# Kernel optimization log

Measured on AMD Instinct MI355X. Metric: run time of the kernel, lower is better.

## Reference

```python
import jax, jax.numpy as jnp
import numpy as np

HEAD_SIZE = 64


def setup_inputs() -> dict:
    key = jax.random.key(0)
    kx, kq, kk, kv = jax.random.split(key, 4)
    B, L, D = 4, 4096, 1024
    scale = 1.0 / np.sqrt(D)
    x = jax.random.normal(kx, (B, L, D), dtype=jnp.float32)
    Wq = jax.random.normal(kq, (D, HEAD_SIZE), dtype=jnp.float32) * scale
    Wk = jax.random.normal(kk, (D, HEAD_SIZE), dtype=jnp.float32) * scale
    Wv = jax.random.normal(kv, (D, HEAD_SIZE), dtype=jnp.float32) * scale
    return {"x": x, "Wq": Wq, "Wk": Wk, "Wv": Wv}


def reference(x, Wq, Wk, Wv):
    B, L, D = x.shape
    H = Wq.shape[1]
    q = jnp.einsum('bld,dh->blh', x, Wq)  # [B,L,H]
    k = jnp.einsum('bld,dh->blh', x, Wk)
    v = jnp.einsum('bld,dh->blh', x, Wv)
    # full L x L score matrix, as in the original module
    scores = jnp.einsum('bqh,bkh->bqk', q, k) / jnp.sqrt(jnp.float32(H))
    causal = jnp.tril(jnp.ones((L, L), dtype=bool))
    scores = jnp.where(causal, scores, -jnp.inf)
    attn = jax.nn.softmax(scores, axis=-1)
    z = jnp.einsum('bqk,bkh->bqh', attn, v)  # [B,L,H]
    return z
```

## Files before the change

### kernel.cpp

```cpp
#include <hip/hip_runtime.h>
#include <stdint.h>

#define L_SEQ 4096
#define D_MODEL 1024
#define HEAD 64
#define CHUNK 512
#define MAXCH 8
#define NQT 128

typedef unsigned short u16;
typedef __attribute__((ext_vector_type(8))) short bf16x8;
typedef __attribute__((ext_vector_type(4))) float f32x4;

static __device__ __forceinline__ u16 f2bf(float f) {
    union { float f; uint32_t u; } c; c.f = f;
    uint32_t u = c.u;
    return (u16)((u + 0x7FFFu + ((u >> 16) & 1u)) >> 16);
}
static __device__ __forceinline__ bf16x8 ld8(const u16* p) { return *(const bf16x8*)p; }

static __device__ __forceinline__ f32x4 mfma16(bf16x8 a, bf16x8 b, f32x4 c) {
    return __builtin_amdgcn_mfma_f32_16x16x32_bf16(a, b, c, 0, 0, 0);
}

__global__ __launch_bounds__(256) void conv_w(
    const float* __restrict__ Wq, const float* __restrict__ Wk,
    const float* __restrict__ Wv, u16* __restrict__ Wt)
{
    __shared__ u16 tile[64][72];
    const float* W = (blockIdx.y == 0) ? Wq : (blockIdx.y == 1) ? Wk : Wv;
    u16* dst = Wt + blockIdx.y * (HEAD * D_MODEL);
    const int k0 = blockIdx.x * 64, t = threadIdx.x;
    #pragma unroll
    for (int i = 0; i < 16; i++) {
        int idx = i * 256 + t;
        int kk = idx >> 6, h = idx & 63;
        tile[h][kk] = f2bf(W[(size_t)(k0 + kk) * HEAD + h]);
    }
    __syncthreads();
    #pragma unroll
    for (int i = 0; i < 16; i++) {
        int idx = i * 256 + t;
        int h = idx >> 6, kk = idx & 63;
        dst[(size_t)h * D_MODEL + k0 + kk] = tile[h][kk];
    }
}

__global__ __launch_bounds__(256) void qkv_proj(
    const float* __restrict__ x, const u16* __restrict__ Wt,
    u16* __restrict__ qb, u16* __restrict__ kb, u16* __restrict__ vTb)
{
    __shared__ __align__(16) char smem[64512];
    u16* WlB = (u16*)smem;
    u16* XlB = (u16*)(smem + 55296);
    u16* CtB = (u16*)smem;
#define WL(bb,r,c) WlB[((bb)*192 + (r))*72 + (c)]
#define XL(bb,r,c) XlB[((bb)*32  + (r))*72 + (c)]
#define CT(r,c)    CtB[(r)*200 + (c)]

    const int t = threadIdx.x;
    const int wv = t >> 6, lane = t & 63;
    const int ln16 = lane & 15, quad = lane >> 4;
    const int w3 = wv * 3;
    const int m0 = blockIdx.x * 32;

    f32x4 acc[2][3] = {};

    auto stage = [&](int s, int bb) {
        const int k0 = s * 64;
        #pragma unroll
        for (int i = 0; i < 6; i++) {
            int idx = i * 256 + t;
            int row = idx >> 3, cg = (idx & 7) * 8;
            bf16x8 wv8 = ld8(&Wt[(size_t)row * D_MODEL + k0 + cg]);
            *(bf16x8*)&WL(bb, row, cg) = wv8;
        }
        #pragma unroll
        for (int i = 0; i < 2; i++) {
            int idx = i * 256 + t;
            int row = idx >> 4, cs = (idx & 15) * 4;
            const float4 xv = *(const float4*)&x[(size_t)(m0 + row) * D_MODEL + k0 + cs];
            uint2 pk;
            pk.x = (uint32_t)f2bf(xv.x) | ((uint32_t)f2bf(xv.y) << 16);
            pk.y = (uint32_t)f2bf(xv.z) | ((uint32_t)f2bf(xv.w) << 16);
            *(uint2*)&XL(bb, row, cs) = pk;
        }
    };

    stage(0, 0);
    int buf = 0;
    for (int s = 0; s < 16; s++) {
        __syncthreads();
        if (s + 1 < 16) stage(s + 1, buf ^ 1);
        #pragma unroll
        for (int c = 0; c < 2; c++) {
            bf16x8 xb0 = ld8(&XL(buf, ln16,      c * 32 + quad * 8));
            bf16x8 xb1 = ld8(&XL(buf, 16 + ln16, c * 32 + quad * 8));
            #pragma unroll
            for (int j = 0; j < 3; j++) {
                bf16x8 af = ld8(&WL(buf, (w3 + j) * 16 + ln16, c * 32 + quad * 8));
                acc[0][j] = mfma16(af, xb0, acc[0][j]);
                acc[1][j] = mfma16(af, xb1, acc[1][j]);
            }
        }
        buf ^= 1;
    }

    __syncthreads();
    #pragma unroll
    for (int mt = 0; mt < 2; mt++) {
        #pragma unroll
        for (int j = 0; j < 3; j++) {
            int g0 = (w3 + j) * 16 + quad * 4;
            float sc = (g0 < 64) ? 0.125f : 1.0f;
            uint2 pk;
            pk.x = (uint32_t)f2bf(acc[mt][j][0] * sc) | ((uint32_t)f2bf(acc[mt][j][1] * sc) << 16);
            pk.y = (uint32_t)f2bf(acc[mt][j][2] * sc) | ((uint32_t)f2bf(acc[mt][j][3] * sc) << 16);
            *(uint2*)&CT(mt * 16 + ln16, g0) = pk;
        }
    }
    __syncthreads();
    {
        int m = t >> 3, hg = (t & 7) * 8;
        *(bf16x8*)&qb[(size_t)(m0 + m) * HEAD + hg] = *(bf16x8*)&CT(m, hg);
        *(bf16x8*)&kb[(size_t)(m0 + m) * HEAD + hg] = *(bf16x8*)&CT(m, 64 + hg);
        int h = t >> 2, mg = (t & 3) * 8;
        bf16x8 vv;
        #pragma unroll
        for (int jj = 0; jj < 8; jj++) vv[jj] = (short)CT(mg + jj, 128 + h);
        int bbt = m0 >> 12, l0 = m0 & 4095;
        *(bf16x8*)&vTb[(size_t)(bbt * HEAD + h) * L_SEQ + l0 + mg] = vv;
    }
#undef WL
#undef XL
#undef CT
}

__global__ __launch_bounds__(256, 2) void attn_chunk(
    const u16* __restrict__ qb, const u16* __restrict__ kb,
    const u16* __restrict__ vT, float* __restrict__ Opart, float* __restrict__ lpart)
{
    const int qt = blockIdx.x, ch = blockIdx.y, b = blockIdx.z;
    if (ch * CHUNK > qt * 32 + 31) return;

    __shared__ __align__(16) char smem[26496];

    const int t = threadIdx.x, wv = t >> 6, lane = t & 63;
    const int ln16 = lane & 15, quad = lane >> 4;
    const int qmin0 = qt * 32;

    u16 (*P)[72] = (u16(*)[72])smem + wv * 32;

    bf16x8 qf[2][2];
    #pragma unroll
    for (int qn = 0; qn < 2; qn++) {
        const u16* qrp = qb + (size_t)(b * L_SEQ + qmin0 + qn * 16 + ln16) * HEAD + quad * 8;
        qf[qn][0] = ld8(qrp); qf[qn][1] = ld8(qrp + 32);
    }

    const u16* kbb = kb + (size_t)b * L_SEQ * HEAD;
    const u16* vbb = vT + (size_t)b * HEAD * L_SEQ;

    f32x4 o[2][4] = {};
    float lsum[2] = {0.f, 0.f};

    const int blk_hi = min(ch * CHUNK + CHUNK, qt * 32 + 32);
    const int kv_lo = ch * CHUNK + wv * 128;
    const int kv_hi = min(kv_lo + 128, blk_hi);
    const bool has0 = kv_lo < kv_hi;
    const bool has1 = kv_lo + 64 < kv_hi;

    bf16x8 K0a[4], K0b[4], V0a[4], V0b[4];
    bf16x8 K1a[4], K1b[4], V1a[4], V1b[4];

    if (has0) {
        #pragma unroll
        for (int g = 0; g < 4; g++) {
            const u16* kr = kbb + (size_t)(kv_lo + g * 16 + ln16) * HEAD + quad * 8;
            K0a[g] = ld8(kr); K0b[g] = ld8(kr + 32);
            const u16* vr = vbb + (size_t)(g * 16 + ln16) * L_SEQ + kv_lo + quad * 8;
            V0a[g] = ld8(vr); V0b[g] = ld8(vr + 32);
        }
    }
    if (has1) {
        #pragma unroll
        for (int g = 0; g < 4; g++) {
            const u16* kr = kbb + (size_t)(kv_lo + 64 + g * 16 + ln16) * HEAD + quad * 8;
            K1a[g] = ld8(kr); K1b[g] = ld8(kr + 32);
            const u16* vr = vbb + (size_t)(g * 16 + ln16) * L_SEQ + kv_lo + 64 + quad * 8;
            V1a[g] = ld8(vr); V1b[g] = ld8(vr + 32);
        }
    }

    auto tile = [&](int kv0, bf16x8* Ka, bf16x8* Kb2, bf16x8* Va, bf16x8* Vb2) {
        #pragma unroll
        for (int g = 0; g < 4; g++) {
            #pragma unroll
            for (int qn = 0; qn < 2; qn++) {
                f32x4 s = {};
                s = mfma16(Ka[g], qf[qn][0], s);
                s = mfma16(Kb2[g], qf[qn][1], s);
                float p0, p1, p2, p3;
                if (kv0 + g * 16 + 15 <= qmin0 + qn * 16) {
                    p0 = __expf(s[0]); p1 = __expf(s[1]);
                    p2 = __expf(s[2]); p3 = __expf(s[3]);
                } else {
                    int q = qmin0 + qn * 16 + ln16;
                    int kv = kv0 + g * 16 + quad * 4;
                    p0 = (kv     <= q) ? __expf(s[0]) : 0.f;
                    p1 = (kv + 1 <= q) ? __expf(s[1]) : 0.f;
                    p2 = (kv + 2 <= q) ? __expf(s[2]) : 0.f;
                    p3 = (kv + 3 <= q) ? __expf(s[3]) : 0.f;
                }
                lsum[qn] += p0 + p1 + p2 + p3;
                uint32_t lo = (uint32_t)f2bf(p0) | ((uint32_t)f2bf(p1) << 16);
                uint32_t hi = (uint32_t)f2bf(p2) | ((uint32_t)f2bf(p3) << 16);
                uint32_t* dst = (uint32_t*)&P[qn * 16 + ln16][g * 16 + quad * 4];
                dst[0] = lo; dst[1] = hi;
            }
        }
        bf16x8 pf0[2], pf1[2];
        #pragma unroll
        for (int qn = 0; qn < 2; qn++) {
            pf0[qn] = ld8(&P[qn * 16 + ln16][quad * 8]);
            pf1[qn] = ld8(&P[qn * 16 + ln16][32 + quad * 8]);
        }
        #pragma unroll
        for (int hg = 0; hg < 4; hg++) {
            #pragma unroll
            for (int qn = 0; qn < 2; qn++) {
                o[qn][hg] = mfma16(Va[hg], pf0[qn], o[qn][hg]);
                o[qn][hg] = mfma16(Vb2[hg], pf1[qn], o[qn][hg]);
            }
        }
    };

    if (has0) tile(kv_lo,      K0a, K0b, V0a, V0b);
    if (has1) tile(kv_lo + 64, K1a, K1b, V1a, V1b);

    #pragma unroll
    for (int qn = 0; qn < 2; qn++) {
        lsum[qn] += __shfl_xor(lsum[qn], 16);
        lsum[qn] += __shfl_xor(lsum[qn], 32);
    }

    __syncthreads();
    float (*cb)[68] = (float(*)[68])smem;
    float* lb = (float*)(smem + 26112);
    if (wv > 0) {
        #pragma unroll
        for (int qn = 0; qn < 2; qn++) {
            #pragma unroll
            for (int hg = 0; hg < 4; hg++)
                *(f32x4*)&cb[(wv - 1) * 32 + qn * 16 + ln16][hg * 16 + quad * 4] = o[qn][hg];
            if (quad == 0) lb[(wv - 1) * 32 + qn * 16 + ln16] = lsum[qn];
        }
    }
    __syncthreads();
    if (wv == 0) {
        const size_t base = (size_t)((b * NQT + qt) * MAXCH + ch);
        #pragma unroll
        for (int qn = 0; qn < 2; qn++) {
            int q = qn * 16 + ln16;
            #pragma unroll
            for (int w2 = 0; w2 < 3; w2++) {
                lsum[qn] += lb[w2 * 32 + q];
                #pragma unroll
                for (int hg = 0; hg < 4; hg++) {
                    f32x4 v = *(f32x4*)&cb[w2 * 32 + q][hg * 16 + quad * 4];
                    o[qn][hg][0] += v[0]; o[qn][hg][1] += v[1];
                    o[qn][hg][2] += v[2]; o[qn][hg][3] += v[3];
                }
            }
            #pragma unroll
            for (int hg = 0; hg < 4; hg++)
                *(f32x4*)&Opart[base * 2048 + (size_t)q * 64 + hg * 16 + quad * 4] = o[qn][hg];
            if (quad == 0)
                lpart[base * 32 + q] = lsum[qn];
        }
    }
}

__global__ __launch_bounds__(256) void merge_chunks(
    const float* __restrict__ Opart, const float* __restrict__ lpart,
    float* __restrict__ out)
{
    const int qt = blockIdx.x, b = blockIdx.y;
    const int nch = qt / 16 + 1;
    const int t = threadIdx.x;
    const size_t obase = (size_t)((b * NQT + qt) * MAXCH) * 2048;
    const size_t lbase = (size_t)((b * NQT + qt) * MAXCH) * 32;
    #pragma unroll
    for (int i = 0; i < 2; i++) {
        int idx = i * 256 + t;
        int q = idx >> 4, hg = (idx & 15) * 4;
        f32x4 vals[MAXCH];
        float ls[MAXCH];
        #pragma unroll
        for (int c = 0; c < MAXCH; c++) {
            vals[c] = *(const f32x4*)&Opart[obase + (size_t)c * 2048 + q * 64 + hg];
            ls[c] = lpart[lbase + c * 32 + q];
        }
        float L = 0.f, ax = 0.f, ay = 0.f, az = 0.f, aw = 0.f;
        #pragma unroll
        for (int c = 0; c < MAXCH; c++) {
            float m = (c < nch) ? 1.f : 0.f;
            L += ls[c] * m;
            ax += vals[c][0] * m; ay += vals[c][1] * m;
            az += vals[c][2] * m; aw += vals[c][3] * m;
        }
        float inv = 1.f / L;
        float4 r; r.x = ax * inv; r.y = ay * inv; r.z = az * inv; r.w = aw * inv;
        *(float4*)&out[((size_t)(b * L_SEQ + qt * 32 + q)) * HEAD + hg] = r;
    }
}

extern "C" void kernel_launch(void* const* d_in, const int* in_sizes, int n_in,
                              void* d_out, int out_size, void* d_ws, size_t ws_size,
                              hipStream_t stream) {
    const float* x  = (const float*)d_in[0];
    const float* Wq = (const float*)d_in[1];
    const float* Wk = (const float*)d_in[2];
    const float* Wv = (const float*)d_in[3];
    float* out = (float*)d_out;

    u16* ws16 = (u16*)d_ws;
    u16* Wt  = ws16;
    u16* qb  = Wt + 3 * HEAD * D_MODEL;
    u16* kb  = qb + 16384 * HEAD;
    u16* vTb = kb + 16384 * HEAD;
    float* Opart = (float*)(vTb + 16384 * HEAD);
    float* lpart = Opart + (size_t)4096 * 2048;

    conv_w      <<<dim3(16, 3), 256, 0, stream>>>(Wq, Wk, Wv, Wt);
    qkv_proj    <<<dim3(512), 256, 0, stream>>>(x, Wt, qb, kb, vTb);
    attn_chunk  <<<dim3(NQT, 8, 4), 256, 0, stream>>>(qb, kb, vTb, Opart, lpart);
    merge_chunks<<<dim3(NQT, 4), 256, 0, stream>>>(Opart, lpart, out);
}
```

Before: 168.4 us.

## Restructure attention to 128-query tiles with async LDS-staged K/V double buffering

The attention kernel now gives each block 128 queries (32 per wave) and streams the 512-key chunk through LDS in double-buffered 64-key stages loaded with global_load_lds. Previously each wave held 128 keys in registers for a 32-query tile and needed a cross-wave reduction. The aim is K/V reuse across four waves and removal of that reduction. The QKV projection also switches its weight staging to async direct-to-LDS loads and overlaps the x loads with the MFMA loop. The cost is more LDS use and barriers per stage, plus a coarser grid of fewer blocks, which may lower occupancy and load balance.

```diff
diff --git a/kernel.cpp b/kernel.cpp
--- a/kernel.cpp
+++ b/kernel.cpp
@@ -6,7 +6,7 @@
 #define HEAD 64
 #define CHUNK 512
 #define MAXCH 8
-#define NQT 128
+#define NQT 32
 
 typedef unsigned short u16;
 typedef __attribute__((ext_vector_type(8))) short bf16x8;
@@ -21,6 +21,12 @@
 
 static __device__ __forceinline__ f32x4 mfma16(bf16x8 a, bf16x8 b, f32x4 c) {
     return __builtin_amdgcn_mfma_f32_16x16x32_bf16(a, b, c, 0, 0, 0);
+}
+
+static __device__ __forceinline__ void gload16(const u16* g, u16* l) {
+    __builtin_amdgcn_global_load_lds(
+        (const __attribute__((address_space(1))) void*)g,
+        (__attribute__((address_space(3))) void*)l, 16, 0, 0);
 }
 
 __global__ __launch_bounds__(256) void conv_w(
@@ -50,13 +56,11 @@
     const float* __restrict__ x, const u16* __restrict__ Wt,
     u16* __restrict__ qb, u16* __restrict__ kb, u16* __restrict__ vTb)
 {
-    __shared__ __align__(16) char smem[64512];
-    u16* WlB = (u16*)smem;
-    u16* XlB = (u16*)(smem + 55296);
-    u16* CtB = (u16*)smem;
-#define WL(bb,r,c) WlB[((bb)*192 + (r))*72 + (c)]
-#define XL(bb,r,c) XlB[((bb)*32  + (r))*72 + (c)]
-#define CT(r,c)    CtB[(r)*200 + (c)]
+    __shared__ __align__(16) u16 Wl[2 * 2 * 192 * 32];
+    __shared__ __align__(16) u16 Xl[2 * 2 * 32 * 36];
+#define WLX(bb,dh,r,c) Wl[(((bb)*2 + (dh))*192 + (r))*32 + (c)]
+#define XLX(bb,kh,r,c) Xl[(((bb)*2 + (kh))*32  + (r))*36 + (c)]
+#define CT(r,c)        ((u16*)Wl)[(r)*200 + (c)]
 
     const int t = threadIdx.x;
     const int wv = t >> 6, lane = t & 63;
@@ -65,44 +69,58 @@
     const int m0 = blockIdx.x * 32;
 
     f32x4 acc[2][3] = {};
-
-    auto stage = [&](int s, int bb) {
+    float4 xv0, xv1;
+
+    auto issueW = [&](int s, int bb) {
         const int k0 = s * 64;
         #pragma unroll
-        for (int i = 0; i < 6; i++) {
-            int idx = i * 256 + t;
-            int row = idx >> 3, cg = (idx & 7) * 8;
-            bf16x8 wv8 = ld8(&Wt[(size_t)row * D_MODEL + k0 + cg]);
-            *(bf16x8*)&WL(bb, row, cg) = wv8;
-        }
-        #pragma unroll
-        for (int i = 0; i < 2; i++) {
-            int idx = i * 256 + t;
-            int row = idx >> 4, cs = (idx & 15) * 4;
-            const float4 xv = *(const float4*)&x[(size_t)(m0 + row) * D_MODEL + k0 + cs];
-            uint2 pk;
-            pk.x = (uint32_t)f2bf(xv.x) | ((uint32_t)f2bf(xv.y) << 16);
-            pk.y = (uint32_t)f2bf(xv.z) | ((uint32_t)f2bf(xv.w) << 16);
-            *(uint2*)&XL(bb, row, cs) = pk;
+        for (int k2 = 0; k2 < 6; k2++) {
+            int c = wv * 6 + k2;
+            int dh = c & 1, g = c >> 1;
+            const u16* gp = Wt + (size_t)(g * 16 + (lane >> 2)) * D_MODEL
+                               + k0 + dh * 32 + (lane & 3) * 8;
+            gload16(gp, &WLX(bb, dh, g * 16 + (lane >> 2), (lane & 3) * 8));
         }
     };
-
-    stage(0, 0);
+    auto loadx = [&](int s) {
+        const int k0 = s * 64;
+        int r0 = t >> 4, cs0 = (t & 15) * 4;
+        xv0 = *(const float4*)&x[(size_t)(m0 + r0) * D_MODEL + k0 + cs0];
+        int idx = 256 + t, r1 = idx >> 4, cs1 = (idx & 15) * 4;
+        xv1 = *(const float4*)&x[(size_t)(m0 + r1) * D_MODEL + k0 + cs1];
+    };
+    auto packx = [&](int bb) {
+        int r0 = t >> 4, cs0 = (t & 15) * 4;
+        uint2 p0;
+        p0.x = (uint32_t)f2bf(xv0.x) | ((uint32_t)f2bf(xv0.y) << 16);
+        p0.y = (uint32_t)f2bf(xv0.z) | ((uint32_t)f2bf(xv0.w) << 16);
+        *(uint2*)&XLX(bb, cs0 >> 5, r0, cs0 & 31) = p0;
+        int idx = 256 + t, r1 = idx >> 4, cs1 = (idx & 15) * 4;
+        uint2 p1;
+        p1.x = (uint32_t)f2bf(xv1.x) | ((uint32_t)f2bf(xv1.y) << 16);
+        p1.y = (uint32_t)f2bf(xv1.z) | ((uint32_t)f2bf(xv1.w) << 16);
+        *(uint2*)&XLX(bb, cs1 >> 5, r1, cs1 & 31) = p1;
+    };
+
+    issueW(0, 0);
+    loadx(0);
+    packx(0);
     int buf = 0;
     for (int s = 0; s < 16; s++) {
         __syncthreads();
-        if (s + 1 < 16) stage(s + 1, buf ^ 1);
+        if (s + 1 < 16) { issueW(s + 1, buf ^ 1); loadx(s + 1); }
         #pragma unroll
         for (int c = 0; c < 2; c++) {
-            bf16x8 xb0 = ld8(&XL(buf, ln16,      c * 32 + quad * 8));
-            bf16x8 xb1 = ld8(&XL(buf, 16 + ln16, c * 32 + quad * 8));
+            bf16x8 xb0 = ld8(&XLX(buf, c, ln16, quad * 8));
+            bf16x8 xb1 = ld8(&XLX(buf, c, 16 + ln16, quad * 8));
             #pragma unroll
             for (int j = 0; j < 3; j++) {
-                bf16x8 af = ld8(&WL(buf, (w3 + j) * 16 + ln16, c * 32 + quad * 8));
+                bf16x8 af = ld8(&WLX(buf, c, (w3 + j) * 16 + ln16, quad * 8));
                 acc[0][j] = mfma16(af, xb0, acc[0][j]);
                 acc[1][j] = mfma16(af, xb1, acc[1][j]);
             }
         }
+        if (s + 1 < 16) packx(buf ^ 1);
         buf ^= 1;
     }
 
@@ -125,36 +143,39 @@
         *(bf16x8*)&qb[(size_t)(m0 + m) * HEAD + hg] = *(bf16x8*)&CT(m, hg);
         *(bf16x8*)&kb[(size_t)(m0 + m) * HEAD + hg] = *(bf16x8*)&CT(m, 64 + hg);
         int h = t >> 2, mg = (t & 3) * 8;
-        bf16x8 vv;
-        #pragma unroll
-        for (int jj = 0; jj < 8; jj++) vv[jj] = (short)CT(mg + jj, 128 + h);
+        bf16x8 vvv;
+        #pragma unroll
+        for (int jj = 0; jj < 8; jj++) vvv[jj] = (short)CT(mg + jj, 128 + h);
         int bbt = m0 >> 12, l0 = m0 & 4095;
-        *(bf16x8*)&vTb[(size_t)(bbt * HEAD + h) * L_SEQ + l0 + mg] = vv;
-    }
-#undef WL
-#undef XL
+        *(bf16x8*)&vTb[(size_t)(bbt * HEAD + h) * L_SEQ + l0 + mg] = vvv;
+    }
+#undef WLX
+#undef XLX
 #undef CT
 }
 
-__global__ __launch_bounds__(256, 2) void attn_chunk(
+__global__ __launch_bounds__(256) void attn_chunk(
     const u16* __restrict__ qb, const u16* __restrict__ kb,
     const u16* __restrict__ vT, float* __restrict__ Opart, float* __restrict__ lpart)
 {
     const int qt = blockIdx.x, ch = blockIdx.y, b = blockIdx.z;
-    if (ch * CHUNK > qt * 32 + 31) return;
-
-    __shared__ __align__(16) char smem[26496];
+    if (ch * CHUNK > qt * 128 + 127) return;
+
+    __shared__ __align__(16) u16 Kls[2 * 2 * 64 * 32];
+    __shared__ __align__(16) u16 Vls[2 * 2 * 64 * 32];
+    __shared__ __align__(16) u16 Pls[4 * 32 * 72];
+#define KBX(bb,dh,r,c) Kls[(((bb)*2 + (dh))*64 + (r))*32 + (c)]
+#define VBX(bb,kh,r,c) Vls[(((bb)*2 + (kh))*64 + (r))*32 + (c)]
+#define PX(r,c)        Pls[((wv)*32 + (r))*72 + (c)]
 
     const int t = threadIdx.x, wv = t >> 6, lane = t & 63;
     const int ln16 = lane & 15, quad = lane >> 4;
-    const int qmin0 = qt * 32;
-
-    u16 (*P)[72] = (u16(*)[72])smem + wv * 32;
+    const int qmin = qt * 128 + wv * 32;
 
     bf16x8 qf[2][2];
     #pragma unroll
     for (int qn = 0; qn < 2; qn++) {
-        const u16* qrp = qb + (size_t)(b * L_SEQ + qmin0 + qn * 16 + ln16) * HEAD + quad * 8;
+        const u16* qrp = qb + (size_t)(b * L_SEQ + qmin + qn * 16 + ln16) * HEAD + quad * 8;
         qf[qn][0] = ld8(qrp); qf[qn][1] = ld8(qrp + 32);
     }
 
@@ -164,79 +185,81 @@
     f32x4 o[2][4] = {};
     float lsum[2] = {0.f, 0.f};
 
-    const int blk_hi = min(ch * CHUNK + CHUNK, qt * 32 + 32);
-    const int kv_lo = ch * CHUNK + wv * 128;
-    const int kv_hi = min(kv_lo + 128, blk_hi);
-    const bool has0 = kv_lo < kv_hi;
-    const bool has1 = kv_lo + 64 < kv_hi;
-
-    bf16x8 K0a[4], K0b[4], V0a[4], V0b[4];
-    bf16x8 K1a[4], K1b[4], V1a[4], V1b[4];
-
-    if (has0) {
+    const int kv_lo = ch * CHUNK;
+    const int kv_hi = min(kv_lo + CHUNK, qt * 128 + 128);
+    const int nst = (kv_hi - kv_lo) >> 6;
+
+    auto issue_stage = [&](int kv0, int bb) {
+        #pragma unroll
+        for (int k2 = 0; k2 < 4; k2++) {
+            int c = wv * 4 + k2;
+            if (c < 8) {
+                int dh = c & 1, g = c >> 1;
+                const u16* gp = kbb + (size_t)(kv0 + g * 16 + (lane >> 2)) * HEAD
+                                    + dh * 32 + (lane & 3) * 8;
+                gload16(gp, &KBX(bb, dh, g * 16 + (lane >> 2), (lane & 3) * 8));
+            } else {
+                int c2 = c - 8, kh = c2 & 1, g = c2 >> 1;
+                const u16* gp = vbb + (size_t)(g * 16 + (lane >> 2)) * L_SEQ
+                                    + kv0 + kh * 32 + (lane & 3) * 8;
+                gload16(gp, &VBX(bb, kh, g * 16 + (lane >> 2), (lane & 3) * 8));
+            }
+        }
+    };
+
+    issue_stage(kv_lo, 0);
+    int buf = 0;
+    for (int s = 0; s < nst; s++) {
+        __syncthreads();
+        if (s + 1 < nst) issue_stage(kv_lo + (s + 1) * 64, buf ^ 1);
+        const int kv0 = kv_lo + s * 64;
+
         #pragma unroll
         for (int g = 0; g < 4; g++) {
-            const u16* kr = kbb + (size_t)(kv_lo + g * 16 + ln16) * HEAD + quad * 8;
-            K0a[g] = ld8(kr); K0b[g] = ld8(kr + 32);
-            const u16* vr = vbb + (size_t)(g * 16 + ln16) * L_SEQ + kv_lo + quad * 8;
-            V0a[g] = ld8(vr); V0b[g] = ld8(vr + 32);
-        }
-    }
-    if (has1) {
-        #pragma unroll
-        for (int g = 0; g < 4; g++) {
-            const u16* kr = kbb + (size_t)(kv_lo + 64 + g * 16 + ln16) * HEAD + quad * 8;
-            K1a[g] = ld8(kr); K1b[g] = ld8(kr + 32);
-            const u16* vr = vbb + (size_t)(g * 16 + ln16) * L_SEQ + kv_lo + 64 + quad * 8;
-            V1a[g] = ld8(vr); V1b[g] = ld8(vr + 32);
-        }
-    }
-
-    auto tile = [&](int kv0, bf16x8* Ka, bf16x8* Kb2, bf16x8* Va, bf16x8* Vb2) {
-        #pragma unroll
-        for (int g = 0; g < 4; g++) {
+            bf16x8 ka0 = ld8(&KBX(buf, 0, g * 16 + ln16, quad * 8));
+            bf16x8 ka1 = ld8(&KBX(buf, 1, g * 16 + ln16, quad * 8));
             #pragma unroll
             for (int qn = 0; qn < 2; qn++) {
-                f32x4 s = {};
-                s = mfma16(Ka[g], qf[qn][0], s);
-                s = mfma16(Kb2[g], qf[qn][1], s);
+                f32x4 s2 = {};
+                s2 = mfma16(ka0, qf[qn][0], s2);
+                s2 = mfma16(ka1, qf[qn][1], s2);
                 float p0, p1, p2, p3;
-                if (kv0 + g * 16 + 15 <= qmin0 + qn * 16) {
-                    p0 = __expf(s[0]); p1 = __expf(s[1]);
-                    p2 = __expf(s[2]); p3 = __expf(s[3]);
+                if (kv0 + g * 16 + 15 <= qmin + qn * 16) {
+                    p0 = __expf(s2[0]); p1 = __expf(s2[1]);
+                    p2 = __expf(s2[2]); p3 = __expf(s2[3]);
                 } else {
-                    int q = qmin0 + qn * 16 + ln16;
+                    int q = qmin + qn * 16 + ln16;
                     int kv = kv0 + g * 16 + quad * 4;
-                    p0 = (kv     <= q) ? __expf(s[0]) : 0.f;
-                    p1 = (kv + 1 <= q) ? __expf(s[1]) : 0.f;
-                    p2 = (kv + 2 <= q) ? __expf(s[2]) : 0.f;
-                    p3 = (kv + 3 <= q) ? __expf(s[3]) : 0.f;
+                    p0 = (kv     <= q) ? __expf(s2[0]) : 0.f;
+                    p1 = (kv + 1 <= q) ? __expf(s2[1]) : 0.f;
+                    p2 = (kv + 2 <= q) ? __expf(s2[2]) : 0.f;
+                    p3 = (kv + 3 <= q) ? __expf(s2[3]) : 0.f;
                 }
                 lsum[qn] += p0 + p1 + p2 + p3;
-                uint32_t lo = (uint32_t)f2bf(p0) | ((uint32_t)f2bf(p1) << 16);
-                uint32_t hi = (uint32_t)f2bf(p2) | ((uint32_t)f2bf(p3) << 16);
-                uint32_t* dst = (uint32_t*)&P[qn * 16 + ln16][g * 16 + quad * 4];
-                dst[0] = lo; dst[1] = hi;
+                uint2 pk;
+                pk.x = (uint32_t)f2bf(p0) | ((uint32_t)f2bf(p1) << 16);
+                pk.y = (uint32_t)f2bf(p2) | ((uint32_t)f2bf(p3) << 16);
+                *(uint2*)&PX(qn * 16 + ln16, g * 16 + quad * 4) = pk;
             }
         }
-        bf16x8 pf0[2], pf1[2];
+        bf16x8 pf[2][2];
         #pragma unroll
         for (int qn = 0; qn < 2; qn++) {
-            pf0[qn] = ld8(&P[qn * 16 + ln16][quad * 8]);
-            pf1[qn] = ld8(&P[qn * 16 + ln16][32 + quad * 8]);
+            pf[qn][0] = ld8(&PX(qn * 16 + ln16, quad * 8));
+            pf[qn][1] = ld8(&PX(qn * 16 + ln16, 32 + quad * 8));
         }
         #pragma unroll
         for (int hg = 0; hg < 4; hg++) {
+            bf16x8 va0 = ld8(&VBX(buf, 0, hg * 16 + ln16, quad * 8));
+            bf16x8 va1 = ld8(&VBX(buf, 1, hg * 16 + ln16, quad * 8));
             #pragma unroll
             for (int qn = 0; qn < 2; qn++) {
-                o[qn][hg] = mfma16(Va[hg], pf0[qn], o[qn][hg]);
-                o[qn][hg] = mfma16(Vb2[hg], pf1[qn], o[qn][hg]);
+                o[qn][hg] = mfma16(va0, pf[qn][0], o[qn][hg]);
+                o[qn][hg] = mfma16(va1, pf[qn][1], o[qn][hg]);
             }
         }
-    };
-
-    if (has0) tile(kv_lo,      K0a, K0b, V0a, V0b);
-    if (has1) tile(kv_lo + 64, K1a, K1b, V1a, V1b);
+        buf ^= 1;
+    }
 
     #pragma unroll
     for (int qn = 0; qn < 2; qn++) {
@@ -244,41 +267,19 @@
         lsum[qn] += __shfl_xor(lsum[qn], 32);
     }
 
-    __syncthreads();
-    float (*cb)[68] = (float(*)[68])smem;
-    float* lb = (float*)(smem + 26112);
-    if (wv > 0) {
-        #pragma unroll
-        for (int qn = 0; qn < 2; qn++) {
-            #pragma unroll
-            for (int hg = 0; hg < 4; hg++)
-                *(f32x4*)&cb[(wv - 1) * 32 + qn * 16 + ln16][hg * 16 + quad * 4] = o[qn][hg];
-            if (quad == 0) lb[(wv - 1) * 32 + qn * 16 + ln16] = lsum[qn];
-        }
-    }
-    __syncthreads();
-    if (wv == 0) {
-        const size_t base = (size_t)((b * NQT + qt) * MAXCH + ch);
-        #pragma unroll
-        for (int qn = 0; qn < 2; qn++) {
-            int q = qn * 16 + ln16;
-            #pragma unroll
-            for (int w2 = 0; w2 < 3; w2++) {
-                lsum[qn] += lb[w2 * 32 + q];
-                #pragma unroll
-                for (int hg = 0; hg < 4; hg++) {
-                    f32x4 v = *(f32x4*)&cb[w2 * 32 + q][hg * 16 + quad * 4];
-                    o[qn][hg][0] += v[0]; o[qn][hg][1] += v[1];
-                    o[qn][hg][2] += v[2]; o[qn][hg][3] += v[3];
-                }
-            }
-            #pragma unroll
-            for (int hg = 0; hg < 4; hg++)
-                *(f32x4*)&Opart[base * 2048 + (size_t)q * 64 + hg * 16 + quad * 4] = o[qn][hg];
-            if (quad == 0)
-                lpart[base * 32 + q] = lsum[qn];
-        }
-    }
+    const size_t base = (size_t)((b * NQT + qt) * MAXCH + ch);
+    #pragma unroll
+    for (int qn = 0; qn < 2; qn++) {
+        int q_local = wv * 32 + qn * 16 + ln16;
+        #pragma unroll
+        for (int hg = 0; hg < 4; hg++)
+            *(f32x4*)&Opart[base * 8192 + (size_t)q_local * 64 + hg * 16 + quad * 4] = o[qn][hg];
+        if (quad == 0)
+            lpart[base * 128 + q_local] = lsum[qn];
+    }
+#undef KBX
+#undef VBX
+#undef PX
 }
 
 __global__ __launch_bounds__(256) void merge_chunks(
@@ -286,20 +287,20 @@
     float* __restrict__ out)
 {
     const int qt = blockIdx.x, b = blockIdx.y;
-    const int nch = qt / 16 + 1;
+    const int nch = qt / 4 + 1;
     const int t = threadIdx.x;
-    const size_t obase = (size_t)((b * NQT + qt) * MAXCH) * 2048;
-    const size_t lbase = (size_t)((b * NQT + qt) * MAXCH) * 32;
-    #pragma unroll
-    for (int i = 0; i < 2; i++) {
+    const size_t obase = (size_t)((b * NQT + qt) * MAXCH) * 8192;
+    const size_t lbase = (size_t)((b * NQT + qt) * MAXCH) * 128;
+    #pragma unroll
+    for (int i = 0; i < 8; i++) {
         int idx = i * 256 + t;
         int q = idx >> 4, hg = (idx & 15) * 4;
         f32x4 vals[MAXCH];
         float ls[MAXCH];
         #pragma unroll
         for (int c = 0; c < MAXCH; c++) {
-            vals[c] = *(const f32x4*)&Opart[obase + (size_t)c * 2048 + q * 64 + hg];
-            ls[c] = lpart[lbase + c * 32 + q];
+            vals[c] = *(const f32x4*)&Opart[obase + (size_t)c * 8192 + q * 64 + hg];
+            ls[c] = lpart[lbase + c * 128 + q];
         }
         float L = 0.f, ax = 0.f, ay = 0.f, az = 0.f, aw = 0.f;
         #pragma unroll
@@ -311,7 +312,7 @@
         }
         float inv = 1.f / L;
         float4 r; r.x = ax * inv; r.y = ay * inv; r.z = az * inv; r.w = aw * inv;
-        *(float4*)&out[((size_t)(b * L_SEQ + qt * 32 + q)) * HEAD + hg] = r;
+        *(float4*)&out[((size_t)(b * L_SEQ + qt * 128 + q)) * HEAD + hg] = r;
     }
 }
 
@@ -330,7 +331,7 @@
     u16* kb  = qb + 16384 * HEAD;
     u16* vTb = kb + 16384 * HEAD;
     float* Opart = (float*)(vTb + 16384 * HEAD);
-    float* lpart = Opart + (size_t)4096 * 2048;
+    float* lpart = Opart + (size_t)1024 * 8192;
 
     conv_w      <<<dim3(16, 3), 256, 0, stream>>>(Wq, Wk, Wv, Wt);
     qkv_proj    <<<dim3(512), 256, 0, stream>>>(x, Wt, qb, kb, vTb);
```

Result: faster. 163.4 us (-3.0%).
